# Kernel tuning notes

Hardware: AMD Instinct MI355X
Metric: run time of the kernel (lower is better)

The kernel has to match this reference:

```python
import jax, jax.numpy as jnp
import numpy as np

H = W = 512                      # image_size=512 hardcoded in nr.Renderer
VIEW_TAN = float(np.tan(30.0 * np.pi / 180.0))  # nr default viewing angle
NEAR = 0.1
BIG = 1e10
CHUNK = 64                       # faces per scan step


def setup_inputs() -> dict:
    key = jax.random.key(0)
    k1, k2, k3, k4 = jax.random.split(key, 4)
    V, F = 2048, 4096
    v = jax.random.normal(k1, (1, V, 3), dtype=jnp.float32)
    # __init__ normalization: center and scale to unit cube
    v_max = v.max(axis=1, keepdims=True)
    v_min = v.min(axis=1, keepdims=True)
    v = (v - (v_max + v_min) / 2.0) / ((v_max - v_min).max() / 2.0)
    faces = jax.random.randint(k2, (1, F, 3), 0, V, dtype=jnp.int32)
    textures = jax.random.uniform(k3, (1, F, 2, 2, 2, 3), dtype=jnp.float32)
    image_ref = jax.random.uniform(k4, (1, 3, H, W), dtype=jnp.float32)
    camera_position = jnp.array([0.0, 0.0, -2.732], dtype=jnp.float32)
    camera_up = jnp.array([0.0, 1.0, 0.0], dtype=jnp.float32)
    return {"vertices": v, "faces": faces, "textures": textures,
            "camera_position": camera_position, "camera_up": camera_up,
            "image_ref": image_ref}


def _normalize(x):
    return x / (jnp.linalg.norm(x) + 1e-12)


def _render(vertices, faces, textures, camera_position, camera_up):
    # --- look_at camera transform (at = origin) ---
    eye = camera_position
    z_axis = _normalize(-eye)                       # forward
    x_axis = _normalize(jnp.cross(_normalize(camera_up), z_axis))
    y_axis = jnp.cross(z_axis, x_axis)
    R = jnp.stack([x_axis, y_axis, z_axis], axis=0)  # rows
    v_cam = (vertices[0] - eye) @ R.T               # [V,3]
    # --- perspective projection to NDC ---
    zc = v_cam[:, 2]
    proj = v_cam[:, :2] / (zc[:, None] * VIEW_TAN + 1e-12)  # [V,2]

    # per-face constant label colors (textures are tiled base colors)
    cols = textures[0].mean(axis=(1, 2, 3))          # [F,3]
    tri_xy = proj[faces[0]]                          # [F,3,2]
    tri_z = zc[faces[0]]                             # [F,3]

    # pixel centers in NDC, row 0 at top (y=+1)
    xs = (jnp.arange(W, dtype=jnp.float32) + 0.5) * 2.0 / W - 1.0
    ys = 1.0 - (jnp.arange(H, dtype=jnp.float32) + 0.5) * 2.0 / H
    xx, yy = jnp.meshgrid(xs, ys)                    # [H,W]
    pix = jnp.stack([xx, yy], axis=-1).reshape(-1, 2)  # [P,2]
    P = pix.shape[0]

    F = tri_xy.shape[0]
    S = F // CHUNK
    chunks = (tri_xy.reshape(S, CHUNK, 3, 2),
              tri_z.reshape(S, CHUNK, 3),
              cols.reshape(S, CHUNK, 3))

    def cross2(a, b):
        return a[..., 0] * b[..., 1] - a[..., 1] * b[..., 0]

    def step(carry, chunk):
        zbuf, color = carry                          # [P], [P,3]
        txy, tz, tc = chunk
        p0, p1, p2 = txy[:, 0], txy[:, 1], txy[:, 2]  # [C,2]
        area = cross2(p1 - p0, p2 - p0)              # [C]
        safe_area = jnp.where(jnp.abs(area) > 1e-8, area, 1.0)
        d = pix[:, None, :]                          # [P,1,2]
        w0 = cross2(p2 - p1, d - p1)                 # [P,C]
        w1 = cross2(p0 - p2, d - p2)
        w2 = cross2(p1 - p0, d - p0)
        s = jnp.sign(area)
        inside = ((w0 * s >= 0) & (w1 * s >= 0) & (w2 * s >= 0)
                  & (jnp.abs(area) > 1e-8))          # [P,C]
        b0, b1, b2 = w0 / safe_area, w1 / safe_area, w2 / safe_area
        z = b0 * tz[:, 0] + b1 * tz[:, 1] + b2 * tz[:, 2]  # [P,C]
        zm = jnp.where(inside & (z > NEAR), z, BIG)
        j = jnp.argmin(zm, axis=1)                   # [P]
        zmin = jnp.take_along_axis(zm, j[:, None], axis=1)[:, 0]
        col = tc[j]                                  # [P,3]
        upd = zmin < zbuf
        zbuf = jnp.where(upd, zmin, zbuf)
        color = jnp.where(upd[:, None], col, color)
        return (zbuf, color), None

    init = (jnp.full((P,), BIG, dtype=jnp.float32),
            jnp.zeros((P, 3), dtype=jnp.float32))
    (zbuf, color), _ = jax.lax.scan(step, init, chunks)
    image = color.reshape(H, W, 3).transpose(2, 0, 1)[None]  # [1,3,H,W]
    return image


def reference(vertices, faces, textures, camera_position, camera_up, image_ref):
    image = _render(vertices, faces, textures, camera_position, camera_up)
    image = image[:, ::-1]  # .flip(dims=[1]) -> channel flip as in source
    loss = jnp.sum((image - image_ref) ** 2)
    return loss
```

## Files before the change

kernel.cpp:

```cpp
#include <hip/hip_runtime.h>

#define IMG_H 512
#define IMG_W 512
#define VIEW_TAN_F 0.57735026918962576451f
#define NEARZ 0.1f
#define BIGF 1e10f

#define TILE 32
#define NTX (IMG_W / TILE)
#define NTILES (NTX * NTX)
#define RSPLITS 32
#define RSHIFT 5
#define MAXSURV 128
#define ZSPLIT 8
#define HXF 0.0625f
#define HYF 0.0625f


__global__ void prep_faces(const float* __restrict__ verts,
                           const int* __restrict__ faces,
                           const float* __restrict__ tex,
                           const float* __restrict__ campos,
                           const float* __restrict__ camup,
                           float4* __restrict__ fd,
                           float* __restrict__ cols,
                           unsigned long long* __restrict__ zbuf,
                           unsigned* __restrict__ zhi,
                           float* __restrict__ out,
                           int F)
{
    int gid = blockIdx.x * blockDim.x + threadIdx.x;

    if (out && gid == 0) out[0] = 0.0f;

    if (zbuf) {
        const int P = IMG_H * IMG_W;
        for (int i = gid; i < P; i += gridDim.x * blockDim.x)
            zbuf[i] = ~0ull;
        if (gid < NTILES)
            zhi[gid] = 0x7F7FFFFFu;
    }

    int f = gid;
    if (f >= F) return;

    float ex = campos[0], ey = campos[1], ez = campos[2];
    float ux = camup[0], uy = camup[1], uz = camup[2];
    float zxv = -ex, zyv = -ey, zzv = -ez;
    float inv = 1.0f / (sqrtf(zxv*zxv + zyv*zyv + zzv*zzv) + 1e-12f);
    zxv *= inv; zyv *= inv; zzv *= inv;
    inv = 1.0f / (sqrtf(ux*ux + uy*uy + uz*uz) + 1e-12f);
    ux *= inv; uy *= inv; uz *= inv;
    float xxv = uy*zzv - uz*zyv;
    float xyv = uz*zxv - ux*zzv;
    float xzv = ux*zyv - uy*zxv;
    inv = 1.0f / (sqrtf(xxv*xxv + xyv*xyv + xzv*xzv) + 1e-12f);
    xxv *= inv; xyv *= inv; xzv *= inv;
    float yxv = zyv*xzv - zzv*xyv;
    float yyv = zzv*xxv - zxv*xzv;
    float yzv = zxv*xyv - zyv*xxv;

    float px_[3], py_[3], pz_[3];
    #pragma unroll
    for (int k = 0; k < 3; ++k) {
        int vi = faces[f*3 + k];
        float vx = verts[vi*3+0] - ex;
        float vy = verts[vi*3+1] - ey;
        float vz = verts[vi*3+2] - ez;
        float cx = xxv*vx + xyv*vy + xzv*vz;
        float cy = yxv*vx + yyv*vy + yzv*vz;
        float cz = zxv*vx + zyv*vy + zzv*vz;
        float denom = cz * VIEW_TAN_F + 1e-12f;
        px_[k] = cx / denom;
        py_[k] = cy / denom;
        pz_[k] = cz;
    }
    float x0 = px_[0], y0 = py_[0];
    float x1 = px_[1], y1 = py_[1];
    float x2 = px_[2], y2 = py_[2];
    float area = (x1-x0)*(y2-y0) - (y1-y0)*(x2-x0);
    bool valid = fabsf(area) > 1e-8f;
    float safe = valid ? area : 1.0f;
    float s = (area > 0.0f) ? 1.0f : -1.0f;

    float A0 = -(y2-y1), B0 = (x2-x1), C0 = (y2-y1)*x1 - (x2-x1)*y1;
    float A1 = -(y0-y2), B1 = (x0-x2), C1 = (y0-y2)*x2 - (x0-x2)*y2;
    float A2 = -(y1-y0), B2 = (x1-x0), C2 = (y1-y0)*x0 - (x1-x0)*y0;

    float invs = 1.0f / safe;
    float Az = (A0*pz_[0] + A1*pz_[1] + A2*pz_[2]) * invs;
    float Bz = (B0*pz_[0] + B1*pz_[1] + B2*pz_[2]) * invs;
    float Cz = (C0*pz_[0] + C1*pz_[1] + C2*pz_[2]) * invs;

    A0 *= s; B0 *= s; C0 *= s;
    A1 *= s; B1 *= s; C1 *= s;
    A2 *= s; B2 *= s; C2 *= s;

    if (!valid) {
        A0 = B0 = A1 = B1 = A2 = B2 = 0.0f;
        C0 = C1 = C2 = -1.0f;
        Az = Bz = 0.0f; Cz = 0.0f;
    }

    fd[f*3+0] = make_float4(A0, B0, C0, A1);
    fd[f*3+1] = make_float4(B1, C1, A2, B2);
    fd[f*3+2] = make_float4(C2, Az, Bz, Cz);

    float c0 = 0.0f, c1 = 0.0f, c2 = 0.0f;
    #pragma unroll
    for (int t = 0; t < 8; ++t) {
        c0 += tex[f*24 + t*3 + 0];
        c1 += tex[f*24 + t*3 + 1];
        c2 += tex[f*24 + t*3 + 2];
    }
    cols[f*3+0] = c0 * 0.125f;
    cols[f*3+1] = c1 * 0.125f;
    cols[f*3+2] = c2 * 0.125f;
}

__global__ __launch_bounds__(256) void zhi_tiles(
    const float4* __restrict__ fd, int F, unsigned* __restrict__ zhi)
{
    int b    = blockIdx.x;
    int sub  = b & (ZSPLIT - 1);
    int tile = b >> 3;
    int tX = tile & (NTX - 1);
    int tY = tile >> 4;
    int tid = threadIdx.x;

    float cx = ((float)(tX * TILE + TILE/2)) * (2.0f / IMG_W) - 1.0f;
    float cy = 1.0f - ((float)(tY * TILE + TILE/2)) * (2.0f / IMG_H);

    int nz = (F + ZSPLIT - 1) / ZSPLIT;
    int f0 = sub * nz;
    int f1 = min(f0 + nz, F);

    float local = BIGF;
    for (int f = f0 + tid; f < f1; f += 256) {
        float4 q0 = fd[3*f + 0];
        float4 q1 = fd[3*f + 1];
        float4 q2 = fd[3*f + 2];
        float m0 = fabsf(q0.x)*HXF + fabsf(q0.y)*HYF;
        float m1 = fabsf(q0.w)*HXF + fabsf(q1.x)*HYF;
        float m2 = fabsf(q1.z)*HXF + fabsf(q1.w)*HYF;
        float e0 = fmaf(q0.x, cx, fmaf(q0.y, cy, q0.z));
        float e1 = fmaf(q0.w, cx, fmaf(q1.x, cy, q1.y));
        float e2 = fmaf(q1.z, cx, fmaf(q1.w, cy, q2.x));
        float zc = fmaf(q2.y, cx, fmaf(q2.z, cy, q2.w));
        float dz = fabsf(q2.y)*HXF + fabsf(q2.z)*HYF;
        float covmin = fminf(fminf(e0 - m0, e1 - m1), e2 - m2);
        if (covmin >= 1e-6f && (zc - dz) > NEARZ)
            local = fminf(local, zc + dz);
    }
    #pragma unroll
    for (int off = 32; off > 0; off >>= 1)
        local = fminf(local, __shfl_down(local, off, 64));

    __shared__ float wmin[4];
    int wid  = tid >> 6;
    int lane = tid & 63;
    if (lane == 0) wmin[wid] = local;
    __syncthreads();
    if (tid == 0) {
        float m = fminf(fminf(wmin[0], wmin[1]), fminf(wmin[2], wmin[3]));
        if (m < BIGF)
            atomicMin(&zhi[tile], __float_as_uint(m));
    }
}

__global__ __launch_bounds__(256) void raster_fused(
    const float4* __restrict__ fd,
    const unsigned* __restrict__ zhi,
    int F,
    unsigned long long* __restrict__ zbuf)
{
    __shared__ float4 sQ[MAXSURV][3];
    __shared__ int    sFi[MAXSURV];
    __shared__ int    sCnt;

    int b     = blockIdx.x;
    int split = b & (RSPLITS - 1);
    int tile  = b >> RSHIFT;
    int tX = tile & (NTX - 1);
    int tY = tile >> 4;
    int tid  = threadIdx.x;
    int lane = tid & 63;

    float cx = ((float)(tX * TILE + TILE/2)) * (2.0f / IMG_W) - 1.0f;
    float cy = 1.0f - ((float)(tY * TILE + TILE/2)) * (2.0f / IMG_H);

    float zHi = __uint_as_float(zhi[tile]) + 1e-4f;

    if (tid == 0) sCnt = 0;
    __syncthreads();

    int nf = F >> RSHIFT;
    for (int it = 0; it < nf; it += 256) {
        int r = it + tid;
        bool keep = false;
        float4 q0, q1, q2;
        int f = split + (r << RSHIFT);
        if (r < nf) {
            q0 = fd[3*f + 0];
            q1 = fd[3*f + 1];
            q2 = fd[3*f + 2];
            float e0 = fmaf(q0.x, cx, fmaf(q0.y, cy, q0.z)) + fabsf(q0.x)*HXF + fabsf(q0.y)*HYF;
            float e1 = fmaf(q0.w, cx, fmaf(q1.x, cy, q1.y)) + fabsf(q0.w)*HXF + fabsf(q1.x)*HYF;
            float e2 = fmaf(q1.z, cx, fmaf(q1.w, cy, q2.x)) + fabsf(q1.z)*HXF + fabsf(q1.w)*HYF;
            float zc = fmaf(q2.y, cx, fmaf(q2.z, cy, q2.w));
            float dz = fabsf(q2.y)*HXF + fabsf(q2.z)*HYF;
            keep = (fminf(fminf(e0, e1), e2) >= -1e-6f) && ((zc - dz) <= zHi);
        }
        unsigned long long mball = __ballot(keep);
        int wb = 0;
        if (lane == 0 && mball) wb = atomicAdd(&sCnt, __popcll(mball));
        wb = __shfl(wb, 0, 64);
        if (keep) {
            int pos = wb + __popcll(mball & ((1ull << lane) - 1ull));
            sQ[pos][0] = q0;
            sQ[pos][1] = q1;
            sQ[pos][2] = q2;
            sFi[pos] = f;
        }
    }
    __syncthreads();
    int n = sCnt;
    if (n == 0) return;

    int colp = tX * TILE + (tid & 31);
    int row0 = tY * TILE + (tid >> 5);
    float x  = ((float)colp + 0.5f) * (2.0f / IMG_W) - 1.0f;
    float y0 = 1.0f - ((float)row0 + 0.5f) * (2.0f / IMG_H);

    float bz[4] = {BIGF, BIGF, BIGF, BIGF};
    int   bi[4] = {-1, -1, -1, -1};

    for (int s = 0; s < n; ++s) {
        float4 p0 = sQ[s][0], p1 = sQ[s][1], p2 = sQ[s][2];
        int fi = sFi[s];
        float w0x = fmaf(p0.x, x, p0.z);
        float w1x = fmaf(p0.w, x, p1.y);
        float w2x = fmaf(p1.z, x, p2.x);
        float zx  = fmaf(p2.y, x, p2.w);
        #pragma unroll
        for (int k = 0; k < 4; ++k) {
            float yk = y0 - (float)k * 0.03125f;
            float w0 = fmaf(p0.y, yk, w0x);
            float w1 = fmaf(p1.x, yk, w1x);
            float w2 = fmaf(p1.w, yk, w2x);
            float z  = fmaf(p2.z, yk, zx);
            bool hit = (fminf(fminf(w0, w1), w2) >= 0.0f) && (z > NEARZ);
            bool better = hit && ((z < bz[k]) || (z == bz[k] && fi < bi[k]));
            if (better) { bz[k] = z; bi[k] = fi; }
        }
    }

    #pragma unroll
    for (int k = 0; k < 4; ++k) {
        if (bi[k] >= 0) {
            int p = (row0 + 8*k) * IMG_W + colp;
            unsigned long long key =
                ((unsigned long long)__float_as_uint(bz[k]) << 32) | (unsigned)bi[k];
            if (key < zbuf[p])
                atomicMin(&zbuf[p], key);
        }
    }
}

__global__ __launch_bounds__(256) void resolve_loss(
    const unsigned long long* __restrict__ zbuf,
    const float* __restrict__ cols,
    const float* __restrict__ imref,
    float* __restrict__ out)
{
    const int HW = IMG_H * IMG_W;
    int base = blockIdx.x * 256 + threadIdx.x;
    float loss = 0.0f;
    #pragma unroll
    for (int q = 0; q < 4; ++q) {
        int p = base + q * (HW / 4);
        unsigned long long key = zbuf[p];
        unsigned idx = (unsigned)(key & 0xffffffffull);
        float r = 0.0f, g = 0.0f, bl = 0.0f;
        if (idx != 0xffffffffu) {
            r  = cols[idx*3 + 0];
            g  = cols[idx*3 + 1];
            bl = cols[idx*3 + 2];
        }
        float d0 = bl - imref[0*HW + p];
        float d1 = g  - imref[1*HW + p];
        float d2 = r  - imref[2*HW + p];
        loss += fmaf(d0, d0, fmaf(d1, d1, d2*d2));
    }

    #pragma unroll
    for (int off = 32; off > 0; off >>= 1)
        loss += __shfl_down(loss, off, 64);

    __shared__ float wsum[4];
    int wid  = threadIdx.x >> 6;
    int lane = threadIdx.x & 63;
    if (lane == 0) wsum[wid] = loss;
    __syncthreads();
    if (threadIdx.x == 0)
        atomicAdd(out, wsum[0] + wsum[1] + wsum[2] + wsum[3]);
}

__global__ __launch_bounds__(256) void raster_loss_mono(
    const float4* __restrict__ fd,
    const float* __restrict__ cols,
    const float* __restrict__ imref,
    float* __restrict__ out, int F)
{
    int p = blockIdx.x * 256 + threadIdx.x;
    int col = p & (IMG_W - 1);
    float x = ((float)col + 0.5f) * (2.0f / IMG_W) - 1.0f;
    float y = 1.0f - ((float)(p >> 9) + 0.5f) * (2.0f / IMG_H);

    float bestz = BIGF;
    int besti = -1;
    for (int f = 0; f < F; ++f) {
        float4 q0 = fd[3*f + 0];
        float4 q1 = fd[3*f + 1];
        float4 q2 = fd[3*f + 2];
        float w0 = fmaf(q0.x, x, fmaf(q0.y, y, q0.z));
        float w1 = fmaf(q0.w, x, fmaf(q1.x, y, q1.y));
        float w2 = fmaf(q1.z, x, fmaf(q1.w, y, q2.x));
        float z  = fmaf(q2.y, x, fmaf(q2.z, y, q2.w));
        bool hit = (w0 >= 0.0f) & (w1 >= 0.0f) & (w2 >= 0.0f) & (z > NEARZ);
        float zm = hit ? z : BIGF;
        if (zm < bestz) { bestz = zm; besti = f; }
    }
    float r = 0.0f, g = 0.0f, bl = 0.0f;
    if (besti >= 0) { r = cols[besti*3]; g = cols[besti*3+1]; bl = cols[besti*3+2]; }
    const int HW = IMG_H * IMG_W;
    float d0 = bl - imref[p], d1 = g - imref[HW+p], d2 = r - imref[2*HW+p];
    float loss = fmaf(d0, d0, fmaf(d1, d1, d2*d2));
    #pragma unroll
    for (int off = 32; off > 0; off >>= 1)
        loss += __shfl_down(loss, off, 64);
    __shared__ float wsum[4];
    int wid = threadIdx.x >> 6, lane = threadIdx.x & 63;
    if (lane == 0) wsum[wid] = loss;
    __syncthreads();
    if (threadIdx.x == 0)
        atomicAdd(out, wsum[0] + wsum[1] + wsum[2] + wsum[3]);
}

extern "C" void kernel_launch(void* const* d_in, const int* in_sizes, int n_in,
                              void* d_out, int out_size, void* d_ws, size_t ws_size,
                              hipStream_t stream)
{
    const float* verts  = (const float*)d_in[0];
    const int*   faces  = (const int*)d_in[1];
    const float* tex    = (const float*)d_in[2];
    const float* campos = (const float*)d_in[3];
    const float* camup  = (const float*)d_in[4];
    const float* imref  = (const float*)d_in[5];
    int F = in_sizes[1] / 3;

    const int P = IMG_H * IMG_W;
    size_t zbytes  = (size_t)P * 8;
    size_t zhiB    = (size_t)NTILES * 4;
    size_t fdbytes = (size_t)F * 3 * sizeof(float4);
    size_t cbytes  = (size_t)F * 3 * sizeof(float);
    float* out = (float*)d_out;

    if (ws_size >= zbytes + zhiB + fdbytes + cbytes &&
        (F % RSPLITS) == 0 && (F >> RSHIFT) <= MAXSURV && (P % 1024) == 0) {
        char* w = (char*)d_ws;
        unsigned long long* zbuf = (unsigned long long*)w;          w += zbytes;
        unsigned* zhi  = (unsigned*)w;                              w += zhiB;
        float4*   fd   = (float4*)w;                                w += fdbytes;
        float*    cols = (float*)w;

        int pgrid = (F + 255)/256 > 512 ? (F + 255)/256 : 512;
        prep_faces<<<pgrid, 256, 0, stream>>>(verts, faces, tex, campos, camup,
                                              fd, cols, zbuf, zhi, out, F);
        zhi_tiles<<<NTILES * ZSPLIT, 256, 0, stream>>>(fd, F, zhi);
        raster_fused<<<NTILES * RSPLITS, 256, 0, stream>>>(fd, zhi, F, zbuf);
        resolve_loss<<<P/1024, 256, 0, stream>>>(zbuf, cols, imref, out);
    } else {
        hipMemsetAsync(d_out, 0, sizeof(float), stream);
        float4* fd   = (float4*)d_ws;
        float*  cols = (float*)((char*)d_ws + fdbytes);
        prep_faces<<<(F + 255)/256, 256, 0, stream>>>(verts, faces, tex, campos, camup, fd, cols,
                                                      (unsigned long long*)nullptr,
                                                      (unsigned*)nullptr,
                                                      (float*)nullptr, F);
        raster_loss_mono<<<P/256, 256, 0, stream>>>(fd, cols, imref, out, F);
    }
}
```

Measured before the change: 99.34 us.

## Vectorize zbuf init and texture loads, double z-bound face split

The zbuf clear now writes 16-byte pairs, and the per-face texture mean reads six float4 loads instead of 24 scalar loads. The zhi_tiles kernel splits faces into 16 slices per tile instead of 8, doubling the block count. These target memory-transaction overhead in the prep kernel and parallelism in the tile z-bound pass, at the cost of more atomics on zhi. The fast-path guard is tightened to require F divisible by RSPLITS*ZSPLIT.

```diff
diff --git a/kernel.cpp b/kernel.cpp
--- a/kernel.cpp
+++ b/kernel.cpp
@@ -12,7 +12,8 @@
 #define RSPLITS 32
 #define RSHIFT 5
 #define MAXSURV 128
-#define ZSPLIT 8
+#define ZSPLIT 16
+#define ZSHIFT 4
 #define HXF 0.0625f
 #define HYF 0.0625f
 
@@ -34,9 +35,10 @@
     if (out && gid == 0) out[0] = 0.0f;
 
     if (zbuf) {
-        const int P = IMG_H * IMG_W;
-        for (int i = gid; i < P; i += gridDim.x * blockDim.x)
-            zbuf[i] = ~0ull;
+        const int P2 = (IMG_H * IMG_W) / 2;
+        ulonglong2* z2 = (ulonglong2*)zbuf;
+        for (int i = gid; i < P2; i += gridDim.x * blockDim.x)
+            z2[i] = make_ulonglong2(~0ull, ~0ull);
         if (gid < NTILES)
             zhi[gid] = 0x7F7FFFFFu;
     }
@@ -106,16 +108,19 @@
     fd[f*3+1] = make_float4(B1, C1, A2, B2);
     fd[f*3+2] = make_float4(C2, Az, Bz, Cz);
 
-    float c0 = 0.0f, c1 = 0.0f, c2 = 0.0f;
-    #pragma unroll
-    for (int t = 0; t < 8; ++t) {
-        c0 += tex[f*24 + t*3 + 0];
-        c1 += tex[f*24 + t*3 + 1];
-        c2 += tex[f*24 + t*3 + 2];
-    }
-    cols[f*3+0] = c0 * 0.125f;
-    cols[f*3+1] = c1 * 0.125f;
-    cols[f*3+2] = c2 * 0.125f;
+    const float4* t4 = reinterpret_cast<const float4*>(tex + (size_t)f * 24);
+    float c[3] = {0.0f, 0.0f, 0.0f};
+    #pragma unroll
+    for (int j = 0; j < 6; ++j) {
+        float4 v = t4[j];
+        c[(4*j + 0) % 3] += v.x;
+        c[(4*j + 1) % 3] += v.y;
+        c[(4*j + 2) % 3] += v.z;
+        c[(4*j + 3) % 3] += v.w;
+    }
+    cols[f*3+0] = c[0] * 0.125f;
+    cols[f*3+1] = c[1] * 0.125f;
+    cols[f*3+2] = c[2] * 0.125f;
 }
 
 __global__ __launch_bounds__(256) void zhi_tiles(
@@ -123,7 +128,7 @@
 {
     int b    = blockIdx.x;
     int sub  = b & (ZSPLIT - 1);
-    int tile = b >> 3;
+    int tile = b >> ZSHIFT;
     int tX = tile & (NTX - 1);
     int tY = tile >> 4;
     int tid = threadIdx.x;
@@ -367,7 +372,8 @@
     float* out = (float*)d_out;
 
     if (ws_size >= zbytes + zhiB + fdbytes + cbytes &&
-        (F % RSPLITS) == 0 && (F >> RSHIFT) <= MAXSURV && (P % 1024) == 0) {
+        (F % (RSPLITS * ZSPLIT)) == 0 && (F >> RSHIFT) <= MAXSURV &&
+        (P % 1024) == 0) {
         char* w = (char*)d_ws;
         unsigned long long* zbuf = (unsigned long long*)w;          w += zbytes;
         unsigned* zhi  = (unsigned*)w;                              w += zhiB;
```

New measurement: 101.3 us. 2.0% more time.
